# Optimization experiments

Measured on AMD Instinct MI355X. Metric: run time of the kernel, lower is better.

The kernel has to match this reference:

```python
import jax, jax.numpy as jnp
import numpy as np

BH, N, C, T = 16, 2048, 64, 64


def setup_inputs() -> dict:
    key = jax.random.key(0)
    k1, k2, k3 = jax.random.split(key, 3)
    q = jax.random.normal(k1, (BH, N, C), dtype=jnp.float32)
    qk = jax.random.normal(k2, (BH, N, N), dtype=jnp.float32)
    # learned positional embedding (1, C, T); random instead of zeros so the
    # gather/interpolation path is numerically non-trivial
    pos_emb = jax.random.normal(k3, (1, C, T), dtype=jnp.float32)
    return {"q": q, "qk": qk, "pos_emb": pos_emb}


def reference(q, qk, pos_emb):
    T_ = pos_emb.shape[-1]
    # gate: g_ij = sigmoid(q_i . k_j)
    G = jax.nn.sigmoid(qk)                                   # (BH, N, N)
    # reverse cumulative sum along last dim: p_ij = sum_{k=j..N-1} g_ik
    P = jnp.flip(jnp.cumsum(jnp.flip(G, axis=-1), axis=-1), axis=-1)
    P = jnp.minimum(P, T_ - 1)                                # clamp(max=T-1)
    P_ceil = jnp.ceil(P).astype(jnp.int32)                    # (BH, N, N)
    P_floor = jnp.floor(P).astype(jnp.int32)
    # E[b, n, t] = q[b, n, :] @ pos_emb[0, :, t]  -> (BH, N, T)
    E = jnp.einsum('bnc,ct->bnt', q, pos_emb[0])
    E_ceil = jnp.take_along_axis(E, P_ceil, axis=-1)          # (BH, N, N)
    E_floor = jnp.take_along_axis(E, P_floor, axis=-1)
    w = P - P_floor
    return w * E_ceil + (1.0 - w) * E_floor
```

## Files before the change

kernel.cpp:

```cpp
#include <hip/hip_runtime.h>

#define NN 2048
#define CC 64
#define TT 64
#define NROWS (16 * 2048)

__global__ __launch_bounds__(256, 4) void e_kernel(
    const float* __restrict__ q,
    const float* __restrict__ pos_emb,
    float* __restrict__ E)
{
    const int lane = threadIdx.x & 63;
    const int wv   = threadIdx.x >> 6;
    const int row  = blockIdx.x * 4 + wv;
    const int urow = __builtin_amdgcn_readfirstlane(row);
    const float* qr = q + (size_t)urow * CC;
    const float* pe = pos_emb + lane;
    float acc0 = 0.f, acc1 = 0.f, acc2 = 0.f, acc3 = 0.f;
#pragma unroll
    for (int c = 0; c < CC; c += 4) {
        acc0 = fmaf(qr[c + 0], pe[(c + 0) * TT], acc0);
        acc1 = fmaf(qr[c + 1], pe[(c + 1) * TT], acc1);
        acc2 = fmaf(qr[c + 2], pe[(c + 2) * TT], acc2);
        acc3 = fmaf(qr[c + 3], pe[(c + 3) * TT], acc3);
    }
    E[(size_t)urow * TT + lane] = (acc0 + acc1) + (acc2 + acc3);
}

__global__ __launch_bounds__(256, 8) void cope_kernel(
    const float* __restrict__ qk,
    const float* __restrict__ E,
    float* __restrict__ out)
{
    const int tid  = threadIdx.x;
    const int lane = tid & 63;
    const int wv   = tid >> 6;
    const int row  = blockIdx.x;

    __shared__ float e_lds[TT];
    __shared__ float wave_tot[4];

    const float4* qk4 = (const float4*)(qk + (size_t)row * NN);
    float4 a0 = qk4[2 * tid];
    float4 a1 = qk4[2 * tid + 1];

    if (tid < 16)
        ((float4*)e_lds)[tid] = ((const float4*)(E + (size_t)row * TT))[tid];

    float g[8];
    g[0] = a0.x; g[1] = a0.y; g[2] = a0.z; g[3] = a0.w;
    g[4] = a1.x; g[5] = a1.y; g[6] = a1.z; g[7] = a1.w;
    float s = 0.f;
#pragma unroll
    for (int k = 0; k < 8; ++k) {
        g[k] = __builtin_amdgcn_rcpf(1.0f + __expf(-g[k]));
        s += g[k];
    }

    float inc = s;
#pragma unroll
    for (int o = 1; o < 64; o <<= 1) {
        float t = __shfl_down(inc, o, 64);
        if (lane + o < 64) inc += t;
    }
    const float X = inc - s;
    if (lane == 0) wave_tot[wv] = inc;

    __syncthreads();

    float W = 0.f;
#pragma unroll
    for (int w2 = 0; w2 < 4; ++w2)
        if (w2 > wv) W += wave_tot[w2];
    const float base = X + W;

    float4 o0, o1;
    if (base >= 63.0f) {
        const float e63 = e_lds[63];
        o0 = make_float4(e63, e63, e63, e63);
        o1 = o0;
    } else {
        float o8[8];
        float run = 0.f;
#pragma unroll
        for (int k = 7; k >= 0; --k) {
            run += g[k];
            float P  = fminf(run + base, 63.0f);
            float fl = floorf(P);
            float w  = P - fl;
            int   i0 = (int)fl;
            int   i1 = min(i0 + 1, 63);
            float ef = e_lds[i0];
            float ec = e_lds[i1];
            o8[k] = fmaf(w, ec - ef, ef);
        }
        o0 = make_float4(o8[0], o8[1], o8[2], o8[3]);
        o1 = make_float4(o8[4], o8[5], o8[6], o8[7]);
    }

    float4* op = (float4*)(out + (size_t)row * NN);
    op[2 * tid]     = o0;
    op[2 * tid + 1] = o1;
}

__global__ __launch_bounds__(256, 4) void cope_fused(
    const float* __restrict__ q,
    const float* __restrict__ qk,
    const float* __restrict__ pos_emb,
    float* __restrict__ out)
{
    const int tid  = threadIdx.x;
    const int lane = tid & 63;
    const int wv   = tid >> 6;
    const int row  = blockIdx.x;

    __shared__ float q_lds[CC];
    __shared__ float e_part[4][TT];
    __shared__ float e_row[TT];
    __shared__ float wave_tot[4];

    const size_t rowN = (size_t)row * NN;
    const float4* qk4 = (const float4*)(qk + rowN);
    float4 v0 = qk4[tid * 2];
    float4 v1 = qk4[tid * 2 + 1];

    if (tid < CC) q_lds[tid] = q[(size_t)row * CC + tid];
    __syncthreads();
    {
        const int t  = tid & 63;
        const int c0 = (tid >> 6) * 16;
        float acc = 0.0f;
#pragma unroll
        for (int cc = 0; cc < 16; ++cc)
            acc = fmaf(q_lds[c0 + cc], pos_emb[(c0 + cc) * TT + t], acc);
        e_part[tid >> 6][t] = acc;
    }
    __syncthreads();
    if (tid < TT)
        e_row[tid] = e_part[0][tid] + e_part[1][tid] + e_part[2][tid] + e_part[3][tid];

    float g[8];
    g[0] = v0.x; g[1] = v0.y; g[2] = v0.z; g[3] = v0.w;
    g[4] = v1.x; g[5] = v1.y; g[6] = v1.z; g[7] = v1.w;
#pragma unroll
    for (int k = 0; k < 8; ++k)
        g[k] = 1.0f / (1.0f + __expf(-g[k]));

    float s = 0.0f;
#pragma unroll
    for (int k = 0; k < 8; ++k) s += g[k];

    float inc = s;
#pragma unroll
    for (int o = 1; o < 64; o <<= 1) {
        float tmp = __shfl_down(inc, o, 64);
        if (lane + o < 64) inc += tmp;
    }
    const float X = inc - s;
    if (lane == 0) wave_tot[wv] = inc;
    __syncthreads();

    float W = 0.0f;
#pragma unroll
    for (int w2 = 0; w2 < 4; ++w2)
        if (w2 > wv) W += wave_tot[w2];
    const float base = X + W;

    float o8[8];
    float run = 0.0f;
#pragma unroll
    for (int k = 7; k >= 0; --k) {
        run += g[k];
        float P  = fminf(run + base, 63.0f);
        float fl = floorf(P);
        float w_ = P - fl;
        int   i0 = (int)fl;
        int   i1 = (int)ceilf(P);
        float ef = e_row[i0];
        float ec = e_row[i1];
        o8[k] = fmaf(w_, ec - ef, ef);
    }

    float4* out4 = (float4*)(out + rowN);
    out4[tid * 2]     = make_float4(o8[0], o8[1], o8[2], o8[3]);
    out4[tid * 2 + 1] = make_float4(o8[4], o8[5], o8[6], o8[7]);
}

extern "C" void kernel_launch(void* const* d_in, const int* in_sizes, int n_in,
                              void* d_out, int out_size, void* d_ws, size_t ws_size,
                              hipStream_t stream) {
    const float* q       = (const float*)d_in[0];
    const float* qk      = (const float*)d_in[1];
    const float* pos_emb = (const float*)d_in[2];
    float* out = (float*)d_out;

    const size_t e_bytes = (size_t)NROWS * TT * sizeof(float);
    if (ws_size >= e_bytes) {
        float* E = (float*)d_ws;
        e_kernel<<<dim3(NROWS / 4), dim3(256), 0, stream>>>(q, pos_emb, E);
        cope_kernel<<<dim3(NROWS), dim3(256), 0, stream>>>(qk, E, out);
    } else {
        cope_fused<<<dim3(NROWS), dim3(256), 0, stream>>>(q, qk, pos_emb, out);
    }
}
```

Before: 120.1 us.

## Process one row per wavefront and make E kernel loop over rows

The main kernel now gives each row to a single 64-lane wavefront, with four rows per block, instead of a full 256-thread block. Each lane handles four 8-element chunks, and the suffix scan uses wave shuffles alone, which removes the block barrier and the cross-wave shared-memory reduction. The E kernel launches fewer blocks and has each wave compute four strided rows. The cost is more registers per thread (32 gate values held live) and lower occupancy from the launch bounds of 4.

Result: slower. 129.4 us (+7.8%).

```diff
diff --git a/kernel.cpp b/kernel.cpp
--- a/kernel.cpp
+++ b/kernel.cpp
@@ -3,7 +3,7 @@
 #define NN 2048
 #define CC 64
 #define TT 64
-#define NROWS (16 * 2048)
+#define NROWS  (16 * 2048)
 
 __global__ __launch_bounds__(256, 4) void e_kernel(
     const float* __restrict__ q,
@@ -12,95 +12,120 @@
 {
     const int lane = threadIdx.x & 63;
     const int wv   = threadIdx.x >> 6;
-    const int row  = blockIdx.x * 4 + wv;
-    const int urow = __builtin_amdgcn_readfirstlane(row);
-    const float* qr = q + (size_t)urow * CC;
-    const float* pe = pos_emb + lane;
-    float acc0 = 0.f, acc1 = 0.f, acc2 = 0.f, acc3 = 0.f;
-#pragma unroll
-    for (int c = 0; c < CC; c += 4) {
-        acc0 = fmaf(qr[c + 0], pe[(c + 0) * TT], acc0);
-        acc1 = fmaf(qr[c + 1], pe[(c + 1) * TT], acc1);
-        acc2 = fmaf(qr[c + 2], pe[(c + 2) * TT], acc2);
-        acc3 = fmaf(qr[c + 3], pe[(c + 3) * TT], acc3);
-    }
-    E[(size_t)urow * TT + lane] = (acc0 + acc1) + (acc2 + acc3);
-}
-
-__global__ __launch_bounds__(256, 8) void cope_kernel(
-    const float* __restrict__ qk,
-    const float* __restrict__ E,
-    float* __restrict__ out)
-{
-    const int tid  = threadIdx.x;
-    const int lane = tid & 63;
-    const int wv   = tid >> 6;
-    const int row  = blockIdx.x;
-
-    __shared__ float e_lds[TT];
-    __shared__ float wave_tot[4];
-
-    const float4* qk4 = (const float4*)(qk + (size_t)row * NN);
-    float4 a0 = qk4[2 * tid];
-    float4 a1 = qk4[2 * tid + 1];
-
-    if (tid < 16)
-        ((float4*)e_lds)[tid] = ((const float4*)(E + (size_t)row * TT))[tid];
-
-    float g[8];
-    g[0] = a0.x; g[1] = a0.y; g[2] = a0.z; g[3] = a0.w;
-    g[4] = a1.x; g[5] = a1.y; g[6] = a1.z; g[7] = a1.w;
-    float s = 0.f;
-#pragma unroll
-    for (int k = 0; k < 8; ++k) {
-        g[k] = __builtin_amdgcn_rcpf(1.0f + __expf(-g[k]));
-        s += g[k];
-    }
-
-    float inc = s;
-#pragma unroll
-    for (int o = 1; o < 64; o <<= 1) {
-        float t = __shfl_down(inc, o, 64);
-        if (lane + o < 64) inc += t;
-    }
-    const float X = inc - s;
-    if (lane == 0) wave_tot[wv] = inc;
-
-    __syncthreads();
-
-    float W = 0.f;
-#pragma unroll
-    for (int w2 = 0; w2 < 4; ++w2)
-        if (w2 > wv) W += wave_tot[w2];
-    const float base = X + W;
-
-    float4 o0, o1;
+    const int wid  = blockIdx.x * 4 + wv;
+#pragma unroll
+    for (int r = 0; r < 4; ++r) {
+        const int row  = wid + r * 8192;
+        const int urow = __builtin_amdgcn_readfirstlane(row);
+        const float* qr = q + (size_t)urow * CC;
+        const float* pe = pos_emb + lane;
+        float acc0 = 0.f, acc1 = 0.f, acc2 = 0.f, acc3 = 0.f;
+#pragma unroll
+        for (int c = 0; c < CC; c += 4) {
+            acc0 = fmaf(qr[c + 0], pe[(c + 0) * TT], acc0);
+            acc1 = fmaf(qr[c + 1], pe[(c + 1) * TT], acc1);
+            acc2 = fmaf(qr[c + 2], pe[(c + 2) * TT], acc2);
+            acc3 = fmaf(qr[c + 3], pe[(c + 3) * TT], acc3);
+        }
+        E[(size_t)urow * TT + lane] = (acc0 + acc1) + (acc2 + acc3);
+    }
+}
+
+__device__ __forceinline__ void interp8(const float* __restrict__ elds,
+                                        const float* __restrict__ g8,
+                                        float base, float4& o0, float4& o1)
+{
     if (base >= 63.0f) {
-        const float e63 = e_lds[63];
+        const float e63 = elds[63];
         o0 = make_float4(e63, e63, e63, e63);
         o1 = o0;
     } else {
-        float o8[8];
+        float r[8];
         float run = 0.f;
 #pragma unroll
         for (int k = 7; k >= 0; --k) {
-            run += g[k];
+            run += g8[k];
             float P  = fminf(run + base, 63.0f);
             float fl = floorf(P);
             float w  = P - fl;
             int   i0 = (int)fl;
             int   i1 = min(i0 + 1, 63);
-            float ef = e_lds[i0];
-            float ec = e_lds[i1];
-            o8[k] = fmaf(w, ec - ef, ef);
+            float ef = elds[i0], ec = elds[i1];
+            r[k] = fmaf(w, ec - ef, ef);
         }
-        o0 = make_float4(o8[0], o8[1], o8[2], o8[3]);
-        o1 = make_float4(o8[4], o8[5], o8[6], o8[7]);
-    }
+        o0 = make_float4(r[0], r[1], r[2], r[3]);
+        o1 = make_float4(r[4], r[5], r[6], r[7]);
+    }
+}
+
+__global__ __launch_bounds__(256, 4) void cope_wave(
+    const float* __restrict__ qk,
+    const float* __restrict__ E,
+    float* __restrict__ out)
+{
+    const int tid  = threadIdx.x;
+    const int lane = tid & 63;
+    const int wv   = tid >> 6;
+    const int row  = blockIdx.x * 4 + wv;
+
+    __shared__ float elds_s[4][TT];
+    float* elds = elds_s[wv];
+
+    const float4* p = (const float4*)(qk + (size_t)row * NN);
+    float4 c0 = p[        2*lane], c1 = p[        2*lane + 1];
+    float4 c2 = p[128   + 2*lane], c3 = p[128   + 2*lane + 1];
+    float4 c4 = p[256   + 2*lane], c5 = p[256   + 2*lane + 1];
+    float4 c6 = p[384   + 2*lane], c7 = p[384   + 2*lane + 1];
+    const float ecur = E[(size_t)row * TT + lane];
+
+    elds[lane] = ecur;
+
+    float g[32];
+    g[ 0]=c0.x; g[ 1]=c0.y; g[ 2]=c0.z; g[ 3]=c0.w;
+    g[ 4]=c1.x; g[ 5]=c1.y; g[ 6]=c1.z; g[ 7]=c1.w;
+    g[ 8]=c2.x; g[ 9]=c2.y; g[10]=c2.z; g[11]=c2.w;
+    g[12]=c3.x; g[13]=c3.y; g[14]=c3.z; g[15]=c3.w;
+    g[16]=c4.x; g[17]=c4.y; g[18]=c4.z; g[19]=c4.w;
+    g[20]=c5.x; g[21]=c5.y; g[22]=c5.z; g[23]=c5.w;
+    g[24]=c6.x; g[25]=c6.y; g[26]=c6.z; g[27]=c6.w;
+    g[28]=c7.x; g[29]=c7.y; g[30]=c7.z; g[31]=c7.w;
+
+    float t0 = 0.f, t1 = 0.f, t2 = 0.f, t3 = 0.f;
+#pragma unroll
+    for (int j = 0; j < 8; ++j) {
+        g[j]      = __builtin_amdgcn_rcpf(1.f + __expf(-g[j]));      t0 += g[j];
+        g[8 + j]  = __builtin_amdgcn_rcpf(1.f + __expf(-g[8 + j]));  t1 += g[8 + j];
+        g[16 + j] = __builtin_amdgcn_rcpf(1.f + __expf(-g[16 + j])); t2 += g[16 + j];
+        g[24 + j] = __builtin_amdgcn_rcpf(1.f + __expf(-g[24 + j])); t3 += g[24 + j];
+    }
+
+    float i0 = t0, i1 = t1, i2 = t2, i3 = t3;
+#pragma unroll
+    for (int o = 1; o < 64; o <<= 1) {
+        float a = __shfl_down(i0, o, 64);
+        float b = __shfl_down(i1, o, 64);
+        float c = __shfl_down(i2, o, 64);
+        float d = __shfl_down(i3, o, 64);
+        if (lane + o < 64) { i0 += a; i1 += b; i2 += c; i3 += d; }
+    }
+    const float T1 = __shfl(i1, 0, 64);
+    const float T2 = __shfl(i2, 0, 64);
+    const float T3 = __shfl(i3, 0, 64);
+    const float base3 = i3 - t3;
+    const float base2 = i2 - t2 + T3;
+    const float base1 = i1 - t1 + T2 + T3;
+    const float base0 = i0 - t0 + T1 + T2 + T3;
 
     float4* op = (float4*)(out + (size_t)row * NN);
-    op[2 * tid]     = o0;
-    op[2 * tid + 1] = o1;
+    float4 o0, o1;
+    interp8(elds, g,      base0, o0, o1);
+    op[        2*lane] = o0;  op[        2*lane + 1] = o1;
+    interp8(elds, g + 8,  base1, o0, o1);
+    op[128   + 2*lane] = o0;  op[128   + 2*lane + 1] = o1;
+    interp8(elds, g + 16, base2, o0, o1);
+    op[256   + 2*lane] = o0;  op[256   + 2*lane + 1] = o1;
+    interp8(elds, g + 24, base3, o0, o1);
+    op[384   + 2*lane] = o0;  op[384   + 2*lane + 1] = o1;
 }
 
 __global__ __launch_bounds__(256, 4) void cope_fused(
@@ -197,8 +222,8 @@
     const size_t e_bytes = (size_t)NROWS * TT * sizeof(float);
     if (ws_size >= e_bytes) {
         float* E = (float*)d_ws;
-        e_kernel<<<dim3(NROWS / 4), dim3(256), 0, stream>>>(q, pos_emb, E);
-        cope_kernel<<<dim3(NROWS), dim3(256), 0, stream>>>(qk, E, out);
+        e_kernel<<<dim3(2048), dim3(256), 0, stream>>>(q, pos_emb, E);
+        cope_wave<<<dim3(NROWS / 4), dim3(256), 0, stream>>>(qk, E, out);
     } else {
         cope_fused<<<dim3(NROWS), dim3(256), 0, stream>>>(q, qk, pos_emb, out);
     }
```
